# Kernel optimization log

Measured on AMD Instinct MI355X. Metric: run time of the kernel, lower is better.

Reference implementation:

```python
import jax, jax.numpy as jnp
import numpy as np

B, T, D, H = 4, 4096, 512, 128
NEG_INF = -1e30  # stand-in for float('-inf'); avoids NaN rows if a row were fully masked


def setup_inputs() -> dict:
    key = jax.random.key(0)
    ks = jax.random.split(key, 7)
    scale = 1.0 / np.sqrt(D)
    x = jax.random.normal(ks[0], (B, T, D), dtype=jnp.float32)
    mask = jnp.tril(jnp.ones((T, T), dtype=jnp.int32))  # causal mask, 0 = masked
    wq = jax.random.normal(ks[1], (D, H), dtype=jnp.float32) * scale
    bq = jax.random.normal(ks[2], (H,), dtype=jnp.float32) * 0.01
    wk = jax.random.normal(ks[3], (D, H), dtype=jnp.float32) * scale
    bk = jax.random.normal(ks[4], (H,), dtype=jnp.float32) * 0.01
    wv = jax.random.normal(ks[5], (D, H), dtype=jnp.float32) * scale
    bv = jax.random.normal(ks[6], (H,), dtype=jnp.float32) * 0.01
    return {"x": x, "mask": mask, "wq": wq, "bq": bq, "wk": wk, "bk": bk, "wv": wv, "bv": bv}


def reference(x, mask, wq, bq, wk, bk, wv, bv):
    # q,k,v: [B,T,H]
    q = jnp.einsum('btd,dh->bth', x, wq) + bq
    k = jnp.einsum('btd,dh->bth', x, wk) + bk
    v = jnp.einsum('btd,dh->bth', x, wv) + bv
    inv_sqrt_h = jnp.float32(1.0 / np.sqrt(H))
    attn = jnp.einsum('bqh,bkh->bqk', q, k) * inv_sqrt_h  # [B,T,T]
    attn = jnp.where(mask == 0, NEG_INF, attn)            # mask [T,T] broadcasts over B
    attn = jax.nn.softmax(attn, axis=-1)
    # dropout is identity in eval mode (reference baseline)
    out = jnp.einsum('bqk,bkh->bqh', attn, v)             # [B,T,H]
    return out
```

## Files before the change

kernel.cpp:

```cpp
#include <hip/hip_runtime.h>


typedef __attribute__((ext_vector_type(8))) short short8;
typedef __attribute__((ext_vector_type(4))) float f32x4;
typedef __attribute__((ext_vector_type(4))) unsigned short us4;
typedef __attribute__((ext_vector_type(4))) unsigned int u32x4;

constexpr int Bc = 4, Tc = 4096, Dc = 512, Hc = 128;

#define DEVI static __device__ __forceinline__

DEVI unsigned short f2bf(float f) {
    unsigned int u = __float_as_uint(f);
    u = (u + 0x7FFFu + ((u >> 16) & 1u)) >> 16;
    return (unsigned short)u;
}
DEVI float bf2f(unsigned short s) { return __uint_as_float(((unsigned int)s) << 16); }
DEVI unsigned int cvtpk(float lo, float hi) {
    unsigned int d;
    asm("v_cvt_pk_bf16_f32 %0, %1, %2" : "=v"(d) : "v"(lo), "v"(hi));
    return d;
}
DEVI int chunk_base(int qi) {
    int g = qi >> 3;
    return qi + 4 * g * (g - 1) + g * (qi - 8 * g);
}
DEVI void glds16(const unsigned short* g, unsigned short* l) {
    typedef unsigned int u32g __attribute__((address_space(1)));
    typedef unsigned int u32l __attribute__((address_space(3)));
    __builtin_amdgcn_global_load_lds((const u32g*)g, (u32l*)l, 16, 0, 0);
}


__global__ void k_prep(const float* __restrict__ wq, const float* __restrict__ wk,
                       const float* __restrict__ wv, const float* __restrict__ x,
                       unsigned short* __restrict__ wF, unsigned short* __restrict__ xbF) {
    const int bid = blockIdx.x, t = threadIdx.x;
    if (bid < 96) {
        int tid = bid * 256 + t;
        int f = tid >> 6, l = tid & 63;
        int n = ((f >> 4) << 4) + (l & 15);
        int d0 = (f & 15) * 32 + (l >> 4) * 8;
        int mat = n >> 7, h = n & 127;
        const float* w = (mat == 0) ? wq : (mat == 1) ? wk : wv;
        unsigned int p[4];
#pragma unroll
        for (int jj = 0; jj < 4; ++jj) {
            float lo = w[(size_t)(d0 + 2 * jj) * Hc + h];
            float hi = w[(size_t)(d0 + 2 * jj + 1) * Hc + h];
            p[jj] = cvtpk(lo, hi);
        }
        *(u32x4*)(wF + (size_t)f * 512 + l * 8) = u32x4{p[0], p[1], p[2], p[3]};
    } else {
        int tid = (bid - 96) * 256 + t;
        int f = tid >> 6, l = tid & 63;
        int row = ((f >> 4) << 4) + (l & 15);
        int col0 = (f & 15) * 32 + (l >> 4) * 8;
        const float* xp = x + (size_t)row * Dc + col0;
        float4 v0 = *(const float4*)xp;
        float4 v1 = *(const float4*)(xp + 4);
        u32x4 pk = {cvtpk(v0.x, v0.y), cvtpk(v0.z, v0.w),
                    cvtpk(v1.x, v1.y), cvtpk(v1.z, v1.w)};
        *(u32x4*)(xbF + (size_t)f * 512 + l * 8) = pk;
    }
}

__global__ __launch_bounds__(256, 4)
void k_qkv(const unsigned short* __restrict__ xbF, const unsigned short* __restrict__ wF,
           const float* __restrict__ bq, const float* __restrict__ bk,
           const float* __restrict__ bv,
           unsigned short* __restrict__ Q, unsigned short* __restrict__ Kf,
           unsigned short* __restrict__ Vf) {
    __shared__ __align__(16) unsigned short AsF[8 * 512];
    __shared__ __align__(16) unsigned short BsF[12 * 512];
    const int t = threadIdx.x;
    const int wave = t >> 6, lane = t & 63, quad = lane >> 4, lr = lane & 15;
    const int wm = wave & 1, wn = wave >> 1;
    const int m0 = (blockIdx.x >> 2) * 64;
    const int n0 = (blockIdx.x & 3) * 96;
    const int afb = (m0 >> 4) * 16;
    const int bfb = (n0 >> 4) * 16;

    f32x4 acc[2][3];
#pragma unroll
    for (int mt = 0; mt < 2; ++mt)
#pragma unroll
        for (int nt = 0; nt < 3; ++nt) acc[mt][nt] = f32x4{0.f, 0.f, 0.f, 0.f};

    for (int kc = 0; kc < 8; ++kc) {
        __syncthreads();
#pragma unroll
        for (int i = 0; i < 2; ++i) {
            int q = wave * 2 + i, mg = q >> 1, sl = q & 1;
            glds16(xbF + ((size_t)(afb + mg * 16 + kc * 2 + sl)) * 512 + lane * 8,
                   &AsF[q * 512]);
        }
#pragma unroll
        for (int i = 0; i < 3; ++i) {
            int p = wave * 3 + i, ng = p >> 1, sl = p & 1;
            glds16(wF + ((size_t)(bfb + ng * 16 + kc * 2 + sl)) * 512 + lane * 8,
                   &BsF[p * 512]);
        }
        __syncthreads();
#pragma unroll
        for (int s = 0; s < 2; ++s) {
            short8 a[2], bfr[3];
#pragma unroll
            for (int mt = 0; mt < 2; ++mt)
                a[mt] = *(const short8*)&AsF[((wm * 2 + mt) * 2 + s) * 512 + lane * 8];
#pragma unroll
            for (int nt = 0; nt < 3; ++nt)
                bfr[nt] = *(const short8*)&BsF[((wn * 3 + nt) * 2 + s) * 512 + lane * 8];
#pragma unroll
            for (int mt = 0; mt < 2; ++mt)
#pragma unroll
                for (int nt = 0; nt < 3; ++nt)
                    acc[mt][nt] = __builtin_amdgcn_mfma_f32_16x16x32_bf16(
                        a[mt], bfr[nt], acc[mt][nt], 0, 0, 0);
        }
    }
    const float rsH = 0.12751743f;
#pragma unroll
    for (int nt = 0; nt < 3; ++nt) {
        int gcol = n0 + wn * 48 + nt * 16 + lr;
        int mat = gcol >> 7, h = gcol & 127;
        const float* bb = (mat == 0) ? bq : (mat == 1) ? bk : bv;
        float bias = bb[h];
#pragma unroll
        for (int mt = 0; mt < 2; ++mt) {
            int grow = m0 + wm * 32 + mt * 16 + quad * 4;
            int b2 = grow >> 12, tb = grow & 4095;
            if (mat == 0) {
#pragma unroll
                for (int r = 0; r < 4; ++r)
                    Q[(size_t)(grow + r) * Hc + h] = f2bf((acc[mt][nt][r] + bias) * rsH);
            } else if (mat == 1) {
                int g = tb >> 4;
                int s = h >> 5, qk = (h >> 3) & 3, j = h & 7;
                unsigned short* kfp = Kf + (((size_t)b2 * 256 + g) * 4 + s) * 512
                                         + qk * 128 + j;
#pragma unroll
                for (int r = 0; r < 4; ++r)
                    kfp[(quad * 4 + r) * 8] = f2bf(acc[mt][nt][r] + bias);
            } else {
                int kt = tb >> 6, s2 = (tb >> 5) & 1, q2 = (tb >> 3) & 3, j0 = tb & 7;
                int ht2 = h >> 4, lr2 = h & 15;
                size_t frag = (((size_t)b2 * 64 + kt) * 2 + s2) * 8 + ht2;
                uint2 p = {cvtpk(acc[mt][nt][0] + bias, acc[mt][nt][1] + bias),
                           cvtpk(acc[mt][nt][2] + bias, acc[mt][nt][3] + bias)};
                *(uint2*)(Vf + frag * 512 + (q2 * 16 + lr2) * 8 + j0) = p;
            }
        }
    }
}

__global__ __launch_bounds__(256, 4)
void k_attn_split(const unsigned short* __restrict__ Q, const unsigned short* __restrict__ Kf,
                  const unsigned short* __restrict__ Vf,
                  unsigned short* __restrict__ Opb, float* __restrict__ Lml) {
    const int gid = blockIdx.x;
    const int b = gid & 3;
    const int s = 287 - (gid >> 2);
    int g = 0;
    while (g < 7 && s >= 4 * (g + 1) * (g + 2)) ++g;
    const int r = s - 4 * g * (g + 1);
    const int qi = 8 * g + r / (g + 1);
    const int c = r % (g + 1);
    const int k0 = c * 8;
    const int kend = min(k0 + 8, qi + 1);

    __shared__ __align__(16) unsigned short KsF[16 * 512];
    __shared__ __align__(16) unsigned short VsF[16 * 512];
    const int t = threadIdx.x;
    const int w = t >> 6, lane = t & 63, quad = lane >> 4, lr = lane & 15;
    const int qrow_g = qi * 64 + w * 16 + lr;
    const size_t base = (size_t)b * Tc * Hc;

    short8 qf[4];
#pragma unroll
    for (int sdx = 0; sdx < 4; ++sdx)
        qf[sdx] = *(const short8*)(Q + base + (size_t)qrow_g * Hc + sdx * 32 + quad * 8);

    f32x4 acc[8];
#pragma unroll
    for (int ht = 0; ht < 8; ++ht) acc[ht] = f32x4{0.f, 0.f, 0.f, 0.f};
    float li = 0.f;

    const int loq = quad & 1;
    const int a0 = ((loq << 1) * 16 + lr) * 4;
    const int a1 = a0 + 64;
    const bool hiq = quad >= 2;

    const unsigned short* KfB = Kf + (size_t)b * 524288 + (w * 4) * 512 + lane * 8;
    const unsigned short* VfB = Vf + (size_t)b * 524288 + (w * 4) * 512 + lane * 8;

    short8 kreg[4], vreg[4];
#pragma unroll
    for (int i = 0; i < 4; ++i) {
        kreg[i] = *(const short8*)(KfB + k0 * 8192 + i * 512);
        vreg[i] = *(const short8*)(VfB + k0 * 8192 + i * 512);
    }

    for (int kt = k0; kt < kend; ++kt) {
        __syncthreads();
        {
            unsigned short* kl = &KsF[(w * 4) * 512 + lane * 8];
            unsigned short* vl = &VsF[(w * 4) * 512 + lane * 8];
#pragma unroll
            for (int i = 0; i < 4; ++i) {
                *(short8*)(kl + i * 512) = kreg[i];
                *(short8*)(vl + i * 512) = vreg[i];
            }
        }
        __syncthreads();
        if (kt + 1 < kend) {
#pragma unroll
            for (int i = 0; i < 4; ++i) {
                kreg[i] = *(const short8*)(KfB + (kt + 1) * 8192 + i * 512);
                vreg[i] = *(const short8*)(VfB + (kt + 1) * 8192 + i * 512);
            }
        }

        f32x4 s4[4];
#pragma unroll
        for (int nt = 0; nt < 4; ++nt) {
            s4[nt] = f32x4{0.f, 0.f, 0.f, 0.f};
            const unsigned short* fb = &KsF[(nt * 4) * 512 + lane * 8];
            short8 kf0 = *(const short8*)(fb);
            short8 kf1 = *(const short8*)(fb + 512);
            short8 kf2 = *(const short8*)(fb + 1024);
            short8 kf3 = *(const short8*)(fb + 1536);
            s4[nt] = __builtin_amdgcn_mfma_f32_16x16x32_bf16(kf0, qf[0], s4[nt], 0, 0, 0);
            s4[nt] = __builtin_amdgcn_mfma_f32_16x16x32_bf16(kf1, qf[1], s4[nt], 0, 0, 0);
            s4[nt] = __builtin_amdgcn_mfma_f32_16x16x32_bf16(kf2, qf[2], s4[nt], 0, 0, 0);
            s4[nt] = __builtin_amdgcn_mfma_f32_16x16x32_bf16(kf3, qf[3], s4[nt], 0, 0, 0);
        }
        if (kt == qi) {
#pragma unroll
            for (int nt = 0; nt < 4; ++nt) {
                int kposb = kt * 64 + nt * 16 + quad * 4;
#pragma unroll
                for (int rr = 0; rr < 4; ++rr)
                    if (kposb + rr > qrow_g) s4[nt][rr] = -1e30f;
            }
        }
#pragma unroll
        for (int nt = 0; nt < 4; ++nt) {
#pragma unroll
            for (int rr = 0; rr < 4; ++rr)
                s4[nt][rr] = __builtin_exp2f(s4[nt][rr] - 17.0f);
            li += s4[nt][0] + s4[nt][1] + s4[nt][2] + s4[nt][3];
        }
        unsigned int wvp[4][2];
#pragma unroll
        for (int nt = 0; nt < 4; ++nt) {
            wvp[nt][0] = cvtpk(s4[nt][0], s4[nt][1]);
            wvp[nt][1] = cvtpk(s4[nt][2], s4[nt][3]);
        }
        unsigned int t0[4], t1[4];
#pragma unroll
        for (int j2 = 0; j2 < 4; ++j2) {
            const int ad = (j2 >> 1) ? a1 : a0;
            const int rp = j2 & 1;
            int p0 = __builtin_amdgcn_ds_bpermute(ad, (int)wvp[0][rp]);
            int p1 = __builtin_amdgcn_ds_bpermute(ad, (int)wvp[1][rp]);
            int q0 = __builtin_amdgcn_ds_bpermute(ad, (int)wvp[2][rp]);
            int q1 = __builtin_amdgcn_ds_bpermute(ad, (int)wvp[3][rp]);
            t0[j2] = (unsigned int)(hiq ? p1 : p0);
            t1[j2] = (unsigned int)(hiq ? q1 : q0);
        }
        union { u32x4 u; short8 s; } u0, u1;
        u0.u = u32x4{t0[0], t0[1], t0[2], t0[3]};
        u1.u = u32x4{t1[0], t1[1], t1[2], t1[3]};
        short8 pfr0 = u0.s;
        short8 pfr1 = u1.s;
#pragma unroll
        for (int ht = 0; ht < 8; ++ht) {
            const unsigned short* vb = &VsF[ht * 512 + lane * 8];
            short8 vf0 = *(const short8*)(vb);
            short8 vf1 = *(const short8*)(vb + 4096);
            acc[ht] = __builtin_amdgcn_mfma_f32_16x16x32_bf16(vf0, pfr0, acc[ht], 0, 0, 0);
            acc[ht] = __builtin_amdgcn_mfma_f32_16x16x32_bf16(vf1, pfr1, acc[ht], 0, 0, 0);
        }
    }
    li += __shfl_xor(li, 16);
    li += __shfl_xor(li, 32);
    const int slot = b * 288 + s;
    unsigned short* Op = Opb + (size_t)slot * 8192 + (size_t)(w * 16 + lr) * 128;
#pragma unroll
    for (int ht = 0; ht < 8; ++ht) {
        uint2 p = {cvtpk(acc[ht][0], acc[ht][1]), cvtpk(acc[ht][2], acc[ht][3])};
        *(uint2*)(Op + ht * 16 + quad * 4) = p;
    }
    if (quad == 0) Lml[(size_t)slot * 64 + w * 16 + lr] = li;
}

__global__ __launch_bounds__(256)
void k_combine(const unsigned short* __restrict__ Opb, const float* __restrict__ Lml,
               float* __restrict__ out) {
    const int bid = blockIdx.x;
    const int g = bid & 3, qi = (bid >> 2) & 63, b = bid >> 8;
    const int nc = (qi >> 3) + 1;
    const int slot0 = b * 288 + chunk_base(qi);
    const int t = threadIdx.x;
    const int row = g * 16 + (t >> 4);
    const int col0 = (t & 15) * 8;

    float lg = 0.f;
    for (int cch = 0; cch < nc; ++cch)
        lg += Lml[(size_t)(slot0 + cch) * 64 + row];
    float inv = 1.0f / lg;

    float o[8];
#pragma unroll
    for (int j = 0; j < 8; ++j) o[j] = 0.f;
    for (int cch = 0; cch < nc; ++cch) {
        uint4 v = *(const uint4*)(Opb + (size_t)(slot0 + cch) * 8192 + row * 128 + col0);
        const unsigned short* e = (const unsigned short*)&v;
#pragma unroll
        for (int k = 0; k < 8; ++k) o[k] += bf2f(e[k]);
    }
    float* dst = out + ((size_t)b * Tc + qi * 64 + row) * Hc + col0;
    float4 v0 = {o[0] * inv, o[1] * inv, o[2] * inv, o[3] * inv};
    float4 v1 = {o[4] * inv, o[5] * inv, o[6] * inv, o[7] * inv};
    *(float4*)dst = v0;
    *(float4*)(dst + 4) = v1;
}

extern "C" void kernel_launch(void* const* d_in, const int* in_sizes, int n_in,
                              void* d_out, int out_size, void* d_ws, size_t ws_size,
                              hipStream_t stream) {
    const float* x  = (const float*)d_in[0];
    const float* wq = (const float*)d_in[2];
    const float* bq = (const float*)d_in[3];
    const float* wk = (const float*)d_in[4];
    const float* bk = (const float*)d_in[5];
    const float* wv = (const float*)d_in[6];
    const float* bv = (const float*)d_in[7];
    float* out = (float*)d_out;

    char* ws = (char*)d_ws;
    unsigned short* wF  = (unsigned short*)ws;
    unsigned short* Qb  = (unsigned short*)(ws + (512ull << 10));
    unsigned short* Kf  = (unsigned short*)(ws + (512ull << 10) + (4ull << 20));
    unsigned short* Vf  = (unsigned short*)(ws + (512ull << 10) + (8ull << 20));
    unsigned short* Opb = (unsigned short*)(ws + (512ull << 10) + (12ull << 20));
    float* Lml = (float*)(ws + (32ull << 20));
    unsigned short* xbF = Opb;

    hipLaunchKernelGGL(k_prep, dim3(4192), dim3(256), 0, stream, wq, wk, wv, x, wF, xbF);
    hipLaunchKernelGGL(k_qkv, dim3(1024), dim3(256), 0, stream, xbF, wF, bq, bk, bv, Qb, Kf, Vf);
    hipLaunchKernelGGL(k_attn_split, dim3(1152), dim3(256), 0, stream, Qb, Kf, Vf, Opb, Lml);
    hipLaunchKernelGGL(k_combine, dim3(1024), dim3(256), 0, stream, Opb, Lml, out);
}
```

Baseline: 181.5 us.

## Fuse split-K combine into attention kernel via last-block atomic counter

Removes the separate combine kernel. Each attention block increments a per-(batch, query-tile) atomic counter after writing its partial output, and the block that arrives last for that tile sums the partial outputs and normalisers and writes the final fp32 rows. The counter is zeroed in the prep kernel. This saves one kernel launch and lets the combine work overlap with other attention blocks, at the cost of threadfences, an atomic per block, and a serial combine tail run by one block per tile.

```diff
diff --git a/kernel.cpp b/kernel.cpp
--- a/kernel.cpp
+++ b/kernel.cpp
@@ -34,8 +34,10 @@
 
 __global__ void k_prep(const float* __restrict__ wq, const float* __restrict__ wk,
                        const float* __restrict__ wv, const float* __restrict__ x,
-                       unsigned short* __restrict__ wF, unsigned short* __restrict__ xbF) {
+                       unsigned short* __restrict__ wF, unsigned short* __restrict__ xbF,
+                       int* __restrict__ cnt) {
     const int bid = blockIdx.x, t = threadIdx.x;
+    if (bid == 0) cnt[t] = 0;
     if (bid < 96) {
         int tid = bid * 256 + t;
         int f = tid >> 6, l = tid & 63;
@@ -157,7 +159,8 @@
 __global__ __launch_bounds__(256, 4)
 void k_attn_split(const unsigned short* __restrict__ Q, const unsigned short* __restrict__ Kf,
                   const unsigned short* __restrict__ Vf,
-                  unsigned short* __restrict__ Opb, float* __restrict__ Lml) {
+                  unsigned short* __restrict__ Opb, float* __restrict__ Lml,
+                  int* __restrict__ cnt, float* __restrict__ out) {
     const int gid = blockIdx.x;
     const int b = gid & 3;
     const int s = 287 - (gid >> 2);
@@ -171,6 +174,7 @@
 
     __shared__ __align__(16) unsigned short KsF[16 * 512];
     __shared__ __align__(16) unsigned short VsF[16 * 512];
+    __shared__ int s_old;
     const int t = threadIdx.x;
     const int w = t >> 6, lane = t & 63, quad = lane >> 4, lr = lane & 15;
     const int qrow_g = qi * 64 + w * 16 + lr;
@@ -293,38 +297,38 @@
         *(uint2*)(Op + ht * 16 + quad * 4) = p;
     }
     if (quad == 0) Lml[(size_t)slot * 64 + w * 16 + lr] = li;
-}
-
-__global__ __launch_bounds__(256)
-void k_combine(const unsigned short* __restrict__ Opb, const float* __restrict__ Lml,
-               float* __restrict__ out) {
-    const int bid = blockIdx.x;
-    const int g = bid & 3, qi = (bid >> 2) & 63, b = bid >> 8;
-    const int nc = (qi >> 3) + 1;
-    const int slot0 = b * 288 + chunk_base(qi);
-    const int t = threadIdx.x;
-    const int row = g * 16 + (t >> 4);
-    const int col0 = (t & 15) * 8;
-
-    float lg = 0.f;
-    for (int cch = 0; cch < nc; ++cch)
-        lg += Lml[(size_t)(slot0 + cch) * 64 + row];
-    float inv = 1.0f / lg;
-
-    float o[8];
-#pragma unroll
-    for (int j = 0; j < 8; ++j) o[j] = 0.f;
-    for (int cch = 0; cch < nc; ++cch) {
-        uint4 v = *(const uint4*)(Opb + (size_t)(slot0 + cch) * 8192 + row * 128 + col0);
-        const unsigned short* e = (const unsigned short*)&v;
-#pragma unroll
-        for (int k = 0; k < 8; ++k) o[k] += bf2f(e[k]);
-    }
-    float* dst = out + ((size_t)b * Tc + qi * 64 + row) * Hc + col0;
-    float4 v0 = {o[0] * inv, o[1] * inv, o[2] * inv, o[3] * inv};
-    float4 v1 = {o[4] * inv, o[5] * inv, o[6] * inv, o[7] * inv};
-    *(float4*)dst = v0;
-    *(float4*)(dst + 4) = v1;
+
+    const int nc = g + 1;
+    __threadfence();
+    __syncthreads();
+    if (t == 0) s_old = atomicAdd(&cnt[b * 64 + qi], 1);
+    __syncthreads();
+    if (s_old % nc == nc - 1) {
+        __threadfence();
+        const int slot0 = b * 288 + chunk_base(qi);
+        for (int u = t; u < 1024; u += 256) {
+            int row = u >> 4, col0 = (u & 15) * 8;
+            float lg = 0.f;
+            for (int cc = 0; cc < nc; ++cc)
+                lg += Lml[(size_t)(slot0 + cc) * 64 + row];
+            float inv = 1.0f / lg;
+            float o[8];
+#pragma unroll
+            for (int j = 0; j < 8; ++j) o[j] = 0.f;
+            for (int cc = 0; cc < nc; ++cc) {
+                uint4 v = *(const uint4*)(Opb + (size_t)(slot0 + cc) * 8192
+                                          + row * 128 + col0);
+                const unsigned short* e = (const unsigned short*)&v;
+#pragma unroll
+                for (int k = 0; k < 8; ++k) o[k] += bf2f(e[k]);
+            }
+            float* dst = out + ((size_t)b * Tc + qi * 64 + row) * Hc + col0;
+            float4 v0 = {o[0] * inv, o[1] * inv, o[2] * inv, o[3] * inv};
+            float4 v1 = {o[4] * inv, o[5] * inv, o[6] * inv, o[7] * inv};
+            *(float4*)dst = v0;
+            *(float4*)(dst + 4) = v1;
+        }
+    }
 }
 
 extern "C" void kernel_launch(void* const* d_in, const int* in_sizes, int n_in,
@@ -346,10 +350,10 @@
     unsigned short* Vf  = (unsigned short*)(ws + (512ull << 10) + (8ull << 20));
     unsigned short* Opb = (unsigned short*)(ws + (512ull << 10) + (12ull << 20));
     float* Lml = (float*)(ws + (32ull << 20));
+    int*   cnt = (int*)(ws + (33ull << 20));
     unsigned short* xbF = Opb;
 
-    hipLaunchKernelGGL(k_prep, dim3(4192), dim3(256), 0, stream, wq, wk, wv, x, wF, xbF);
+    hipLaunchKernelGGL(k_prep, dim3(4192), dim3(256), 0, stream, wq, wk, wv, x, wF, xbF, cnt);
     hipLaunchKernelGGL(k_qkv, dim3(1024), dim3(256), 0, stream, xbF, wF, bq, bk, bv, Qb, Kf, Vf);
-    hipLaunchKernelGGL(k_attn_split, dim3(1152), dim3(256), 0, stream, Qb, Kf, Vf, Opb, Lml);
-    hipLaunchKernelGGL(k_combine, dim3(1024), dim3(256), 0, stream, Opb, Lml, out);
-}
+    hipLaunchKernelGGL(k_attn_split, dim3(1152), dim3(256), 0, stream, Qb, Kf, Vf, Opb, Lml, cnt, out);
+}
```

Result: slower. 397.6 us (+119.1%).
